# Performance work log

Measured on AMD Instinct MI355X. Metric: run time of the kernel, lower is better.

## Reference

```python
import jax, jax.numpy as jnp
import numpy as np

N = 100000      # nodes
E = 1600000     # edges
C_IN = 128
H = 64          # hidden_channels
FC = [128, 64, 32, 16]
G = 64          # graphs in batch
EPS = 1e-5


def _glorot(key, fan_in, fan_out):
    s = 1.0 / np.sqrt(fan_in)
    return jax.random.uniform(key, (fan_in, fan_out), jnp.float32, -s, s)


def setup_inputs() -> dict:
    key = jax.random.key(0)
    ks = jax.random.split(key, 24)
    inp = {
        "x": jax.random.normal(ks[0], (N, C_IN), jnp.float32),
        "edge_index": jax.random.randint(ks[1], (2, E), 0, N, jnp.int32),
        "batch": jnp.sort(jax.random.randint(ks[2], (N,), 0, G, jnp.int32)),
        # GCN layers
        "W1": _glorot(ks[3], C_IN, H), "b1": jnp.zeros((H,), jnp.float32),
        "W2": _glorot(ks[4], H, H),    "b2": jnp.zeros((H,), jnp.float32),
        # BatchNorm affine params
        "gamma1": jnp.ones((H,), jnp.float32), "beta1": jnp.zeros((H,), jnp.float32),
        "gamma2": jnp.ones((H,), jnp.float32), "beta2": jnp.zeros((H,), jnp.float32),
        # MLP stack 64->128->64->32->16->1
        "fW1": _glorot(ks[5], H, FC[0]),     "fb1": jnp.zeros((FC[0],), jnp.float32),
        "fW2": _glorot(ks[6], FC[0], FC[1]), "fb2": jnp.zeros((FC[1],), jnp.float32),
        "fW3": _glorot(ks[7], FC[1], FC[2]), "fb3": jnp.zeros((FC[2],), jnp.float32),
        "fW4": _glorot(ks[8], FC[2], FC[3]), "fb4": jnp.zeros((FC[3],), jnp.float32),
        "oW": _glorot(ks[9], FC[3], 1),      "ob": jnp.zeros((1,), jnp.float32),
    }
    return inp


def gcn_conv(x, W, b, src, dst):
    # x' = D^{-1/2} (A + I) D^{-1/2} X W + b   (PyG GCNConv, add_self_loops=True)
    h = x @ W                                             # [N, H]
    loops = jnp.arange(N, dtype=src.dtype)
    s = jnp.concatenate([src, loops])
    d = jnp.concatenate([dst, loops])
    deg = jax.ops.segment_sum(jnp.ones_like(d, jnp.float32), d, num_segments=N)
    dinv = jax.lax.rsqrt(deg)                             # deg >= 1 (self-loops)
    norm = dinv[s] * dinv[d]                              # [E+N]
    msg = h[s] * norm[:, None]                            # gather + scale
    return jax.ops.segment_sum(msg, d, num_segments=N) + b


def batch_norm(x, gamma, beta):
    mu = jnp.mean(x, axis=0)
    var = jnp.mean((x - mu) ** 2, axis=0)                 # biased, as torch BN
    return (x - mu) * jax.lax.rsqrt(var + EPS) * gamma + beta


def reference(x, edge_index, batch, W1, b1, W2, b2, gamma1, beta1, gamma2, beta2,
              fW1, fb1, fW2, fb2, fW3, fb3, fW4, fb4, oW, ob):
    src, dst = edge_index[0], edge_index[1]
    h = jax.nn.relu(gcn_conv(x, W1, b1, src, dst))
    h = batch_norm(h, gamma1, beta1)                      # dropout = identity (eval)
    h = jax.nn.relu(gcn_conv(h, W2, b2, src, dst))
    h = batch_norm(h, gamma2, beta2)
    # global mean pool over graphs
    sums = jax.ops.segment_sum(h, batch, num_segments=G)
    cnts = jax.ops.segment_sum(jnp.ones((N,), jnp.float32), batch, num_segments=G)
    g = sums / jnp.maximum(cnts, 1.0)[:, None]            # [G, H]
    g = jax.nn.relu(g @ fW1 + fb1)
    g = jax.nn.relu(g @ fW2 + fb2)
    g = jax.nn.relu(g @ fW3 + fb3)
    g = jax.nn.relu(g @ fW4 + fb4)
    return g @ oW + ob                                    # [G, 1]
```

## Files before the change

kernel.cpp:

```cpp
#include <hip/hip_runtime.h>
#include <hip/hip_bf16.h>
#include <hip/hip_fp16.h>

#define NNODES 100000
#define NEDGES 1600000
#define NGRAPH 64
#define NCOPY  32
#define NSLOT  8

#define CAP     48
#define NGEMM1  1563

#define PSH     9
#define PSZ2    512
#define NP2     196
#define PCAP    9216
#define EPB     4096
#define NBP1    391

__global__ __launch_bounds__(1024) void k_bucket(const int* __restrict__ ei,
                                                 unsigned* __restrict__ pstage,
                                                 unsigned* __restrict__ pcur) {
    const int tid = threadIdx.x;
    __shared__ unsigned lcnt[NP2];
    __shared__ unsigned lbase[NP2];
    if (tid < NP2) lcnt[tid] = 0u;
    __syncthreads();

    int e = blockIdx.x * EPB + tid * 4;
    bool valid = (e < NEDGES);
    unsigned v0=0,v1=0,v2=0,v3=0, p0=0,p1=0,p2=0,p3=0, o0=0,o1=0,o2=0,o3=0;
    if (valid) {
        int4 sv = *reinterpret_cast<const int4*>(&ei[e]);
        int4 dv = *reinterpret_cast<const int4*>(&ei[NEDGES + e]);
        unsigned d;
        d = (unsigned)dv.x; p0 = d >> PSH; v0 = ((d & (PSZ2-1u)) << 17) | (unsigned)sv.x; o0 = atomicAdd(&lcnt[p0], 1u);
        d = (unsigned)dv.y; p1 = d >> PSH; v1 = ((d & (PSZ2-1u)) << 17) | (unsigned)sv.y; o1 = atomicAdd(&lcnt[p1], 1u);
        d = (unsigned)dv.z; p2 = d >> PSH; v2 = ((d & (PSZ2-1u)) << 17) | (unsigned)sv.z; o2 = atomicAdd(&lcnt[p2], 1u);
        d = (unsigned)dv.w; p3 = d >> PSH; v3 = ((d & (PSZ2-1u)) << 17) | (unsigned)sv.w; o3 = atomicAdd(&lcnt[p3], 1u);
    }
    __syncthreads();
    if (tid < NP2) {
        unsigned c = lcnt[tid];
        lbase[tid] = c ? atomicAdd(&pcur[tid], c) : 0u;
    }
    __syncthreads();
    if (valid) {
        unsigned i0 = lbase[p0] + o0; if (i0 < PCAP) pstage[(size_t)p0 * PCAP + i0] = v0;
        unsigned i1 = lbase[p1] + o1; if (i1 < PCAP) pstage[(size_t)p1 * PCAP + i1] = v1;
        unsigned i2 = lbase[p2] + o2; if (i2 < PCAP) pstage[(size_t)p2 * PCAP + i2] = v2;
        unsigned i3 = lbase[p3] + o3; if (i3 < PCAP) pstage[(size_t)p3 * PCAP + i3] = v3;
    }
}

__global__ __launch_bounds__(1024) void k_build(const unsigned* __restrict__ pstage,
                                                const unsigned* __restrict__ pcur,
                                                unsigned* __restrict__ cnt,
                                                float* __restrict__ dinv,
                                                unsigned* __restrict__ colidx) {
    const int p   = blockIdx.x;
    const int tid = threadIdx.x;
    __shared__ unsigned cl[PSZ2];
    if (tid < PSZ2) cl[tid] = 0u;
    __syncthreads();
    unsigned nedge = min(pcur[p], (unsigned)PCAP);
    const unsigned* q = &pstage[(size_t)p * PCAP];
    for (unsigned i = tid; i < nedge; i += 1024) {
        unsigned v    = q[i];
        unsigned r    = v >> 17;
        unsigned src  = v & 0x1FFFFu;
        unsigned slot = atomicAdd(&cl[r], 1u);
        unsigned node = ((unsigned)p << PSH) + r;
        if (slot < CAP) colidx[node * CAP + slot] = src;
    }
    __syncthreads();
    if (tid < PSZ2) {
        unsigned node = ((unsigned)p << PSH) + (unsigned)tid;
        if (node < NNODES) {
            unsigned c = cl[tid];
            cnt[node]  = c;
            dinv[node] = rsqrtf((float)(c + 1u));
        }
    }
}

__global__ __launch_bounds__(256) void k_gemm1(const float* __restrict__ A,
                                               const float* __restrict__ W,
                                               const float* __restrict__ rowscale,
                                               __half* __restrict__ hd) {
    __shared__ float wlds[64 * 64];
    __shared__ float alds[64 * 68];
    const int tid = threadIdx.x;
    const int tc = (tid & 15) * 4;
    const int tr = (tid >> 4) * 4;
    const int row0 = blockIdx.x * 64;
    float acc[4][4];
    #pragma unroll
    for (int i = 0; i < 4; ++i)
        #pragma unroll
        for (int j = 0; j < 4; ++j) acc[i][j] = 0.f;

    for (int kc = 0; kc < 2; ++kc) {
        for (int idx2 = tid; idx2 < 64 * 16; idx2 += 256) {
            int r = idx2 >> 4, kk = (idx2 & 15) * 4;
            *reinterpret_cast<float4*>(&wlds[r * 64 + kk]) =
                *reinterpret_cast<const float4*>(&W[(kc * 64 + r) * 64 + kk]);
        }
        for (int idx2 = tid; idx2 < 64 * 16; idx2 += 256) {
            int r = idx2 >> 4, kk = (idx2 & 15) * 4;
            int row = row0 + r;
            float4 v = make_float4(0.f, 0.f, 0.f, 0.f);
            if (row < NNODES) v = *reinterpret_cast<const float4*>(&A[(size_t)row * 128 + kc * 64 + kk]);
            *reinterpret_cast<float4*>(&alds[r * 68 + kk]) = v;
        }
        __syncthreads();
        #pragma unroll 8
        for (int k = 0; k < 64; ++k) {
            float4 wv = *reinterpret_cast<const float4*>(&wlds[k * 64 + tc]);
            float av[4];
            #pragma unroll
            for (int i = 0; i < 4; ++i) av[i] = alds[(tr + i) * 68 + k];
            #pragma unroll
            for (int i = 0; i < 4; ++i) {
                acc[i][0] = fmaf(av[i], wv.x, acc[i][0]);
                acc[i][1] = fmaf(av[i], wv.y, acc[i][1]);
                acc[i][2] = fmaf(av[i], wv.z, acc[i][2]);
                acc[i][3] = fmaf(av[i], wv.w, acc[i][3]);
            }
        }
        __syncthreads();
    }
    #pragma unroll
    for (int i = 0; i < 4; ++i) {
        int row = row0 + tr + i;
        if (row < NNODES) {
            float f = rowscale[row];
            __half2* p = reinterpret_cast<__half2*>(&hd[(size_t)row * 64 + tc]);
            p[0] = __floats2half2_rn(acc[i][0] * f, acc[i][1] * f);
            p[1] = __floats2half2_rn(acc[i][2] * f, acc[i][3] * f);
        }
    }
}

__device__ __forceinline__ void acc_row(const __half* __restrict__ hd, unsigned s, int c0, float4& acc) {
    uint2 u = *reinterpret_cast<const uint2*>(&hd[(size_t)s * 64 + c0]);
    __half2 x01 = *reinterpret_cast<__half2*>(&u.x);
    __half2 x23 = *reinterpret_cast<__half2*>(&u.y);
    float2 f01 = __half22float2(x01);
    float2 f23 = __half22float2(x23);
    acc.x += f01.x; acc.y += f01.y; acc.z += f23.x; acc.w += f23.y;
}

#define WAVE_REDUCE_8(s0,s1,s2,s3,q0,q1,q2,q3)                      \
    {                                                                \
        _Pragma("unroll")                                            \
        for (int m = 16; m < 64; m <<= 1) {                          \
            s0 += __shfl_xor(s0, m); s1 += __shfl_xor(s1, m);        \
            s2 += __shfl_xor(s2, m); s3 += __shfl_xor(s3, m);        \
            q0 += __shfl_xor(q0, m); q1 += __shfl_xor(q1, m);        \
            q2 += __shfl_xor(q2, m); q3 += __shfl_xor(q3, m);        \
        }                                                            \
    }

__global__ __launch_bounds__(256) void k_gather_fused(const unsigned* __restrict__ cnt,
                                                      const unsigned* __restrict__ colidx,
                                                      const __half* __restrict__ hd,
                                                      const float* __restrict__ dinv,
                                                      const float* __restrict__ bias,
                                                      __half* __restrict__ acth,
                                                      float* bn_sum, float* bn_sq, int n) {
    const int tid = threadIdx.x;
    const int grp = tid >> 4;
    const int c0  = (tid & 15) * 4;
    float4 bv = *reinterpret_cast<const float4*>(&bias[c0]);
    float s0=0.f,s1=0.f,s2=0.f,s3=0.f, q0=0.f,q1=0.f,q2=0.f,q3=0.f;

    #pragma unroll
    for (int it = 0; it < 2; ++it) {
        int node = blockIdx.x * 32 + grp * 2 + it;
        if (node < n) {
            unsigned deg = cnt[node];
            unsigned lo = (unsigned)node * CAP;
            unsigned hi = lo + deg;
            float4 acc = make_float4(0.f, 0.f, 0.f, 0.f);
            acc_row(hd, (unsigned)node, c0, acc);
            unsigned j = lo;
            for (; j + 4 <= hi; j += 4) {
                uint4 a = *reinterpret_cast<const uint4*>(&colidx[j]);
                acc_row(hd, a.x, c0, acc);
                acc_row(hd, a.y, c0, acc);
                acc_row(hd, a.z, c0, acc);
                acc_row(hd, a.w, c0, acc);
            }
            for (; j < hi; ++j) acc_row(hd, colidx[j], c0, acc);
            float w = dinv[node];
            float4 r;
            r.x = fmaxf(fmaf(acc.x, w, bv.x), 0.f);
            r.y = fmaxf(fmaf(acc.y, w, bv.y), 0.f);
            r.z = fmaxf(fmaf(acc.z, w, bv.z), 0.f);
            r.w = fmaxf(fmaf(acc.w, w, bv.w), 0.f);
            __half2* pa = reinterpret_cast<__half2*>(&acth[(size_t)node * 64 + c0]);
            pa[0] = __floats2half2_rn(r.x, r.y);
            pa[1] = __floats2half2_rn(r.z, r.w);
            s0 += r.x; s1 += r.y; s2 += r.z; s3 += r.w;
            q0 = fmaf(r.x, r.x, q0); q1 = fmaf(r.y, r.y, q1);
            q2 = fmaf(r.z, r.z, q2); q3 = fmaf(r.w, r.w, q3);
        }
    }

    WAVE_REDUCE_8(s0,s1,s2,s3,q0,q1,q2,q3);
    __shared__ float ls[4 * 64];
    __shared__ float lq[4 * 64];
    int lane = tid & 63, wid = tid >> 6;
    if (lane < 16) {
        *reinterpret_cast<float4*>(&ls[wid * 64 + lane * 4]) = make_float4(s0, s1, s2, s3);
        *reinterpret_cast<float4*>(&lq[wid * 64 + lane * 4]) = make_float4(q0, q1, q2, q3);
    }
    __syncthreads();
    if (tid < 64) {
        int cpy = (blockIdx.x & (NCOPY - 1)) * 64;
        float S = ls[tid] + ls[64 + tid] + ls[128 + tid] + ls[192 + tid];
        float Q = lq[tid] + lq[64 + tid] + lq[128 + tid] + lq[192 + tid];
        atomicAdd(&bn_sum[cpy + tid], S);
        atomicAdd(&bn_sq[cpy + tid],  Q);
    }
}

__global__ __launch_bounds__(256) void k_gemm2_fold(const __half* __restrict__ A,
                                                    const float* __restrict__ W2,
                                                    const float* __restrict__ bn_sum,
                                                    const float* __restrict__ bn_sq,
                                                    const float* __restrict__ gamma,
                                                    const float* __restrict__ beta,
                                                    const float* __restrict__ rowscale,
                                                    __half* __restrict__ hd, int n) {
    __shared__ float wlds[64 * 64];
    __shared__ float alds[64 * 68];
    __shared__ float scs[64], shs[64], c2s[64];
    const int tid = threadIdx.x;
    const int tc  = (tid & 15) * 4;
    const int tr  = (tid >> 4) * 4;
    const int row0 = blockIdx.x * 64;

    if (tid < 64) {
        float S = 0.f, Q = 0.f;
        #pragma unroll
        for (int cpy = 0; cpy < NCOPY; ++cpy) { S += bn_sum[cpy * 64 + tid]; Q += bn_sq[cpy * 64 + tid]; }
        float inv_n = 1.0f / (float)n;
        float mu  = S * inv_n;
        float var = Q * inv_n - mu * mu;
        float s = gamma[tid] * rsqrtf(var + 1e-5f);
        scs[tid] = s; shs[tid] = beta[tid] - mu * s;
    }
    __syncthreads();
    for (int idx = tid; idx < 4096; idx += 256) {
        int k = idx >> 6;
        wlds[idx] = scs[k] * W2[idx];
    }
    if (tid < 64) {
        float acc = 0.f;
        for (int k = 0; k < 64; ++k) acc = fmaf(shs[k], W2[k * 64 + tid], acc);
        c2s[tid] = acc;
    }
    for (int idx = tid; idx < 64 * 16; idx += 256) {
        int r = idx >> 4, kk = (idx & 15) * 4;
        int row = row0 + r;
        float4 v = make_float4(0.f, 0.f, 0.f, 0.f);
        if (row < n) {
            uint2 u = *reinterpret_cast<const uint2*>(&A[(size_t)row * 64 + kk]);
            __half2 h01 = *reinterpret_cast<__half2*>(&u.x);
            __half2 h23 = *reinterpret_cast<__half2*>(&u.y);
            float2 f01 = __half22float2(h01);
            float2 f23 = __half22float2(h23);
            v = make_float4(f01.x, f01.y, f23.x, f23.y);
        }
        *reinterpret_cast<float4*>(&alds[r * 68 + kk]) = v;
    }
    __syncthreads();

    float acc[4][4];
    float4 cv = make_float4(c2s[tc], c2s[tc + 1], c2s[tc + 2], c2s[tc + 3]);
    #pragma unroll
    for (int i = 0; i < 4; ++i) { acc[i][0]=cv.x; acc[i][1]=cv.y; acc[i][2]=cv.z; acc[i][3]=cv.w; }

    #pragma unroll 8
    for (int k = 0; k < 64; ++k) {
        float4 wv = *reinterpret_cast<const float4*>(&wlds[k * 64 + tc]);
        float av[4];
        #pragma unroll
        for (int i = 0; i < 4; ++i) av[i] = alds[(tr + i) * 68 + k];
        #pragma unroll
        for (int i = 0; i < 4; ++i) {
            acc[i][0] = fmaf(av[i], wv.x, acc[i][0]);
            acc[i][1] = fmaf(av[i], wv.y, acc[i][1]);
            acc[i][2] = fmaf(av[i], wv.z, acc[i][2]);
            acc[i][3] = fmaf(av[i], wv.w, acc[i][3]);
        }
    }
    #pragma unroll
    for (int i = 0; i < 4; ++i) {
        int row = row0 + tr + i;
        if (row < n) {
            float f = rowscale[row];
            __half2* p = reinterpret_cast<__half2*>(&hd[(size_t)row * 64 + tc]);
            p[0] = __floats2half2_rn(acc[i][0] * f, acc[i][1] * f);
            p[1] = __floats2half2_rn(acc[i][2] * f, acc[i][3] * f);
        }
    }
}

__global__ __launch_bounds__(256) void k_gather_pool(const unsigned* __restrict__ cnt,
                                                     const unsigned* __restrict__ colidx,
                                                     const __half* __restrict__ hd,
                                                     const float* __restrict__ dinv,
                                                     const float* __restrict__ bias,
                                                     const int* __restrict__ batch,
                                                     float* __restrict__ gsum,
                                                     float* bn_sum, float* bn_sq, int n) {
    const int tid = threadIdx.x;
    const int grp = tid >> 4;
    const int c0  = (tid & 15) * 4;
    float4 bv = *reinterpret_cast<const float4*>(&bias[c0]);
    float s0=0.f,s1=0.f,s2=0.f,s3=0.f, q0=0.f,q1=0.f,q2=0.f,q3=0.f;

    __shared__ float lds_pool[NSLOT * 64];
    for (int i = tid; i < NSLOT * 64; i += 256) lds_pool[i] = 0.f;
    int node0 = blockIdx.x * 32;
    int g0 = batch[node0 < n ? node0 : (n - 1)];
    __syncthreads();

    #pragma unroll
    for (int it = 0; it < 2; ++it) {
        int node = node0 + grp * 2 + it;
        if (node < n) {
            unsigned deg = cnt[node];
            unsigned lo = (unsigned)node * CAP;
            unsigned hi = lo + deg;
            float4 acc = make_float4(0.f, 0.f, 0.f, 0.f);
            acc_row(hd, (unsigned)node, c0, acc);
            unsigned j = lo;
            for (; j + 4 <= hi; j += 4) {
                uint4 a = *reinterpret_cast<const uint4*>(&colidx[j]);
                acc_row(hd, a.x, c0, acc);
                acc_row(hd, a.y, c0, acc);
                acc_row(hd, a.z, c0, acc);
                acc_row(hd, a.w, c0, acc);
            }
            for (; j < hi; ++j) acc_row(hd, colidx[j], c0, acc);
            float w = dinv[node];
            float4 r;
            r.x = fmaxf(fmaf(acc.x, w, bv.x), 0.f);
            r.y = fmaxf(fmaf(acc.y, w, bv.y), 0.f);
            r.z = fmaxf(fmaf(acc.z, w, bv.z), 0.f);
            r.w = fmaxf(fmaf(acc.w, w, bv.w), 0.f);
            s0 += r.x; s1 += r.y; s2 += r.z; s3 += r.w;
            q0 = fmaf(r.x, r.x, q0); q1 = fmaf(r.y, r.y, q1);
            q2 = fmaf(r.z, r.z, q2); q3 = fmaf(r.w, r.w, q3);
            int slot = batch[node] - g0;
            if (slot < NSLOT) {
                atomicAdd(&lds_pool[slot * 64 + c0 + 0], r.x);
                atomicAdd(&lds_pool[slot * 64 + c0 + 1], r.y);
                atomicAdd(&lds_pool[slot * 64 + c0 + 2], r.z);
                atomicAdd(&lds_pool[slot * 64 + c0 + 3], r.w);
            } else {
                int g = g0 + slot;
                atomicAdd(&gsum[g * 64 + c0 + 0], r.x);
                atomicAdd(&gsum[g * 64 + c0 + 1], r.y);
                atomicAdd(&gsum[g * 64 + c0 + 2], r.z);
                atomicAdd(&gsum[g * 64 + c0 + 3], r.w);
            }
        }
    }

    WAVE_REDUCE_8(s0,s1,s2,s3,q0,q1,q2,q3);
    __shared__ float ls[4 * 64];
    __shared__ float lq[4 * 64];
    int lane = tid & 63, wid = tid >> 6;
    if (lane < 16) {
        *reinterpret_cast<float4*>(&ls[wid * 64 + lane * 4]) = make_float4(s0, s1, s2, s3);
        *reinterpret_cast<float4*>(&lq[wid * 64 + lane * 4]) = make_float4(q0, q1, q2, q3);
    }
    __syncthreads();
    if (tid < 64) {
        int cpy = (blockIdx.x & (NCOPY - 1)) * 64;
        float S = ls[tid] + ls[64 + tid] + ls[128 + tid] + ls[192 + tid];
        float Q = lq[tid] + lq[64 + tid] + lq[128 + tid] + lq[192 + tid];
        atomicAdd(&bn_sum[cpy + tid], S);
        atomicAdd(&bn_sq[cpy + tid],  Q);
        #pragma unroll
        for (int sl = 0; sl < NSLOT; ++sl) {
            int g = g0 + sl;
            if (g < NGRAPH) {
                float v = lds_pool[sl * 64 + tid];
                if (v != 0.f) atomicAdd(&gsum[g * 64 + tid], v);
            }
        }
    }
}

__device__ __forceinline__ int lower_bound_i(const int* a, int n, int v) {
    int lo = 0, hi = n;
    while (lo < hi) { int m = (lo + hi) >> 1; if (a[m] < v) lo = m + 1; else hi = m; }
    return lo;
}
__global__ __launch_bounds__(128) void k_mlp(const float* __restrict__ gsum,
                                             const int* __restrict__ batch, int n,
                                             const float* __restrict__ bn_sum, const float* __restrict__ bn_sq,
                                             const float* __restrict__ gamma, const float* __restrict__ beta,
                                             const float* __restrict__ fW1, const float* __restrict__ fb1,
                                             const float* __restrict__ fW2, const float* __restrict__ fb2,
                                             const float* __restrict__ fW3, const float* __restrict__ fb3,
                                             const float* __restrict__ fW4, const float* __restrict__ fb4,
                                             const float* __restrict__ oW,  const float* __restrict__ ob,
                                             float* __restrict__ out) {
    int g = blockIdx.x;
    int t = threadIdx.x;
    __shared__ float a[128], bbuf[128];
    if (t < 64) {
        float S = 0.f, Q = 0.f;
        #pragma unroll
        for (int cpy = 0; cpy < NCOPY; ++cpy) { S += bn_sum[cpy * 64 + t]; Q += bn_sq[cpy * 64 + t]; }
        float inv_n = 1.0f / (float)n;
        float mu  = S * inv_n;
        float var = Q * inv_n - mu * mu;
        float s   = gamma[t] * rsqrtf(var + 1e-5f);
        float sh  = beta[t] - mu * s;
        int lo = lower_bound_i(batch, n, g);
        int hi = lower_bound_i(batch, n, g + 1);
        int cnt = hi - lo;
        a[t] = (cnt > 0) ? (gsum[g * 64 + t] / (float)cnt) * s + sh : 0.f;
    }
    __syncthreads();
    {
        float acc = fb1[t];
        for (int k = 0; k < 64; ++k) acc = fmaf(a[k], fW1[k * 128 + t], acc);
        bbuf[t] = fmaxf(acc, 0.f);
    }
    __syncthreads();
    if (t < 64) {
        float acc = fb2[t];
        for (int k = 0; k < 128; ++k) acc = fmaf(bbuf[k], fW2[k * 64 + t], acc);
        a[t] = fmaxf(acc, 0.f);
    }
    __syncthreads();
    if (t < 32) {
        float acc = fb3[t];
        for (int k = 0; k < 64; ++k) acc = fmaf(a[k], fW3[k * 32 + t], acc);
        bbuf[t] = fmaxf(acc, 0.f);
    }
    __syncthreads();
    if (t < 16) {
        float acc = fb4[t];
        for (int k = 0; k < 32; ++k) acc = fmaf(bbuf[k], fW4[k * 16 + t], acc);
        a[t] = fmaxf(acc, 0.f);
    }
    __syncthreads();
    if (t == 0) {
        float acc = ob[0];
        for (int k = 0; k < 16; ++k) acc = fmaf(a[k], oW[k], acc);
        out[g] = acc;
    }
}

extern "C" void kernel_launch(void* const* d_in, const int* in_sizes, int n_in,
                              void* d_out, int out_size, void* d_ws, size_t ws_size,
                              hipStream_t stream) {
    const float* x      = (const float*)d_in[0];
    const int*   ei     = (const int*)  d_in[1];
    const int*   batch  = (const int*)  d_in[2];
    const float* W1     = (const float*)d_in[3];
    const float* b1     = (const float*)d_in[4];
    const float* W2     = (const float*)d_in[5];
    const float* b2     = (const float*)d_in[6];
    const float* gamma1 = (const float*)d_in[7];
    const float* beta1  = (const float*)d_in[8];
    const float* gamma2 = (const float*)d_in[9];
    const float* beta2  = (const float*)d_in[10];
    const float* fW1    = (const float*)d_in[11];
    const float* fb1    = (const float*)d_in[12];
    const float* fW2    = (const float*)d_in[13];
    const float* fb2    = (const float*)d_in[14];
    const float* fW3    = (const float*)d_in[15];
    const float* fb3    = (const float*)d_in[16];
    const float* fW4    = (const float*)d_in[17];
    const float* fb4    = (const float*)d_in[18];
    const float* oW     = (const float*)d_in[19];
    const float* ob     = (const float*)d_in[20];
    float* out = (float*)d_out;

    const int N = NNODES, G = NGRAPH;

    char* base = (char*)d_ws;
    __half*   hd     = (__half*)base;
    __half*   acth   = (__half*)(base + (size_t)N * 64 * 2);
    unsigned* cnt    = (unsigned*)(base + (size_t)N * 64 * 4);
    float*    dinv   = (float*)(cnt + N);
    unsigned* colidx = (unsigned*)(dinv + N);
    float*    bn1s   = (float*)(colidx + (size_t)N * CAP);
    float*    bn1q   = bn1s + NCOPY * 64;
    float*    bn2s   = bn1q + NCOPY * 64;
    float*    bn2q   = bn2s + NCOPY * 64;
    float*    gsum   = bn2q + NCOPY * 64;
    unsigned* pcur   = (unsigned*)(gsum + (size_t)G * 64);
    const size_t ZBYTES = (size_t)(4 * NCOPY * 64 + G * 64) * 4 + (size_t)NP2 * 4;
    unsigned* pstage = (unsigned*)acth;

    hipMemsetAsync(bn1s, 0, ZBYTES, stream);

    k_bucket<<<NBP1, 1024, 0, stream>>>(ei, pstage, pcur);

    k_build<<<NP2, 1024, 0, stream>>>(pstage, pcur, cnt, dinv, colidx);

    k_gemm1<<<NGEMM1, 256, 0, stream>>>(x, W1, dinv, hd);

    k_gather_fused<<<(N + 31) / 32, 256, 0, stream>>>(cnt, colidx, hd, dinv, b1, acth, bn1s, bn1q, N);

    k_gemm2_fold<<<NGEMM1, 256, 0, stream>>>(acth, W2, bn1s, bn1q, gamma1, beta1, dinv, hd, N);

    k_gather_pool<<<(N + 31) / 32, 256, 0, stream>>>(cnt, colidx, hd, dinv, b2, batch, gsum, bn2s, bn2q, N);

    k_mlp<<<G, 128, 0, stream>>>(gsum, batch, N, bn2s, bn2q, gamma2, beta2,
                                 fW1, fb1, fW2, fb2, fW3, fb3, fW4, fb4, oW, ob, out);
}
```

Baseline: 305.9 us.

## Merge memset, bucketing, CSR build and first GEMM into one cooperative kernel

Replaces the memset plus three separate launches (edge bucketing, per-partition CSR build, first-layer GEMM) with a single cooperative kernel that uses grid-wide syncs between phases and grid-stride loops. The zeroing of accumulators moves into the kernel. The GEMM phase is reworked for 1024-thread blocks, with each thread computing one row by four columns instead of a 4x4 tile. This is meant to remove launch gaps and memset overhead, at the cost of grid.sync barriers, lower per-thread GEMM reuse, and occupancy-limited grid sizing.

Result: slower. 654.7 us (+114.0%).

```diff
diff --git a/kernel.cpp b/kernel.cpp
--- a/kernel.cpp
+++ b/kernel.cpp
@@ -1,6 +1,9 @@
 #include <hip/hip_runtime.h>
+#include <hip/hip_cooperative_groups.h>
 #include <hip/hip_bf16.h>
 #include <hip/hip_fp16.h>
+
+namespace cg = cooperative_groups;
 
 #define NNODES 100000
 #define NEDGES 1600000
@@ -18,126 +21,123 @@
 #define EPB     4096
 #define NBP1    391
 
-__global__ __launch_bounds__(1024) void k_bucket(const int* __restrict__ ei,
-                                                 unsigned* __restrict__ pstage,
-                                                 unsigned* __restrict__ pcur) {
-    const int tid = threadIdx.x;
+__global__ __launch_bounds__(1024, 8) void k_front(const float* __restrict__ A,
+                                                   const float* __restrict__ W,
+                                                   const int* __restrict__ ei,
+                                                   unsigned* __restrict__ pstage,
+                                                   unsigned* __restrict__ pcur,
+                                                   unsigned* __restrict__ cnt,
+                                                   float* __restrict__ dinv,
+                                                   unsigned* __restrict__ colidx,
+                                                   float* __restrict__ zbase,
+                                                   int zwords,
+                                                   __half* __restrict__ hd) {
+    cg::grid_group grid = cg::this_grid();
+    const int tid  = threadIdx.x;
+    const int gdim = gridDim.x;
+
     __shared__ unsigned lcnt[NP2];
     __shared__ unsigned lbase[NP2];
-    if (tid < NP2) lcnt[tid] = 0u;
-    __syncthreads();
-
-    int e = blockIdx.x * EPB + tid * 4;
-    bool valid = (e < NEDGES);
-    unsigned v0=0,v1=0,v2=0,v3=0, p0=0,p1=0,p2=0,p3=0, o0=0,o1=0,o2=0,o3=0;
-    if (valid) {
-        int4 sv = *reinterpret_cast<const int4*>(&ei[e]);
-        int4 dv = *reinterpret_cast<const int4*>(&ei[NEDGES + e]);
-        unsigned d;
-        d = (unsigned)dv.x; p0 = d >> PSH; v0 = ((d & (PSZ2-1u)) << 17) | (unsigned)sv.x; o0 = atomicAdd(&lcnt[p0], 1u);
-        d = (unsigned)dv.y; p1 = d >> PSH; v1 = ((d & (PSZ2-1u)) << 17) | (unsigned)sv.y; o1 = atomicAdd(&lcnt[p1], 1u);
-        d = (unsigned)dv.z; p2 = d >> PSH; v2 = ((d & (PSZ2-1u)) << 17) | (unsigned)sv.z; o2 = atomicAdd(&lcnt[p2], 1u);
-        d = (unsigned)dv.w; p3 = d >> PSH; v3 = ((d & (PSZ2-1u)) << 17) | (unsigned)sv.w; o3 = atomicAdd(&lcnt[p3], 1u);
-    }
-    __syncthreads();
-    if (tid < NP2) {
-        unsigned c = lcnt[tid];
-        lbase[tid] = c ? atomicAdd(&pcur[tid], c) : 0u;
-    }
-    __syncthreads();
-    if (valid) {
-        unsigned i0 = lbase[p0] + o0; if (i0 < PCAP) pstage[(size_t)p0 * PCAP + i0] = v0;
-        unsigned i1 = lbase[p1] + o1; if (i1 < PCAP) pstage[(size_t)p1 * PCAP + i1] = v1;
-        unsigned i2 = lbase[p2] + o2; if (i2 < PCAP) pstage[(size_t)p2 * PCAP + i2] = v2;
-        unsigned i3 = lbase[p3] + o3; if (i3 < PCAP) pstage[(size_t)p3 * PCAP + i3] = v3;
-    }
-}
-
-__global__ __launch_bounds__(1024) void k_build(const unsigned* __restrict__ pstage,
-                                                const unsigned* __restrict__ pcur,
-                                                unsigned* __restrict__ cnt,
-                                                float* __restrict__ dinv,
-                                                unsigned* __restrict__ colidx) {
-    const int p   = blockIdx.x;
-    const int tid = threadIdx.x;
     __shared__ unsigned cl[PSZ2];
-    if (tid < PSZ2) cl[tid] = 0u;
-    __syncthreads();
-    unsigned nedge = min(pcur[p], (unsigned)PCAP);
-    const unsigned* q = &pstage[(size_t)p * PCAP];
-    for (unsigned i = tid; i < nedge; i += 1024) {
-        unsigned v    = q[i];
-        unsigned r    = v >> 17;
-        unsigned src  = v & 0x1FFFFu;
-        unsigned slot = atomicAdd(&cl[r], 1u);
-        unsigned node = ((unsigned)p << PSH) + r;
-        if (slot < CAP) colidx[node * CAP + slot] = src;
-    }
-    __syncthreads();
-    if (tid < PSZ2) {
-        unsigned node = ((unsigned)p << PSH) + (unsigned)tid;
-        if (node < NNODES) {
-            unsigned c = cl[tid];
-            cnt[node]  = c;
-            dinv[node] = rsqrtf((float)(c + 1u));
-        }
-    }
-}
-
-__global__ __launch_bounds__(256) void k_gemm1(const float* __restrict__ A,
-                                               const float* __restrict__ W,
-                                               const float* __restrict__ rowscale,
-                                               __half* __restrict__ hd) {
     __shared__ float wlds[64 * 64];
     __shared__ float alds[64 * 68];
-    const int tid = threadIdx.x;
-    const int tc = (tid & 15) * 4;
-    const int tr = (tid >> 4) * 4;
-    const int row0 = blockIdx.x * 64;
-    float acc[4][4];
-    #pragma unroll
-    for (int i = 0; i < 4; ++i)
-        #pragma unroll
-        for (int j = 0; j < 4; ++j) acc[i][j] = 0.f;
-
-    for (int kc = 0; kc < 2; ++kc) {
-        for (int idx2 = tid; idx2 < 64 * 16; idx2 += 256) {
-            int r = idx2 >> 4, kk = (idx2 & 15) * 4;
-            *reinterpret_cast<float4*>(&wlds[r * 64 + kk]) =
-                *reinterpret_cast<const float4*>(&W[(kc * 64 + r) * 64 + kk]);
-        }
-        for (int idx2 = tid; idx2 < 64 * 16; idx2 += 256) {
-            int r = idx2 >> 4, kk = (idx2 & 15) * 4;
-            int row = row0 + r;
-            float4 v = make_float4(0.f, 0.f, 0.f, 0.f);
-            if (row < NNODES) v = *reinterpret_cast<const float4*>(&A[(size_t)row * 128 + kc * 64 + kk]);
-            *reinterpret_cast<float4*>(&alds[r * 68 + kk]) = v;
-        }
-        __syncthreads();
-        #pragma unroll 8
-        for (int k = 0; k < 64; ++k) {
-            float4 wv = *reinterpret_cast<const float4*>(&wlds[k * 64 + tc]);
-            float av[4];
-            #pragma unroll
-            for (int i = 0; i < 4; ++i) av[i] = alds[(tr + i) * 68 + k];
-            #pragma unroll
-            for (int i = 0; i < 4; ++i) {
-                acc[i][0] = fmaf(av[i], wv.x, acc[i][0]);
-                acc[i][1] = fmaf(av[i], wv.y, acc[i][1]);
-                acc[i][2] = fmaf(av[i], wv.z, acc[i][2]);
-                acc[i][3] = fmaf(av[i], wv.w, acc[i][3]);
-            }
-        }
-        __syncthreads();
-    }
-    #pragma unroll
-    for (int i = 0; i < 4; ++i) {
-        int row = row0 + tr + i;
-        if (row < NNODES) {
-            float f = rowscale[row];
-            __half2* p = reinterpret_cast<__half2*>(&hd[(size_t)row * 64 + tc]);
-            p[0] = __floats2half2_rn(acc[i][0] * f, acc[i][1] * f);
-            p[1] = __floats2half2_rn(acc[i][2] * f, acc[i][3] * f);
+
+    for (int i = blockIdx.x * 1024 + tid; i < zwords; i += gdim * 1024) zbase[i] = 0.f;
+    grid.sync();
+
+    for (int s = blockIdx.x; s < NBP1; s += gdim) {
+        if (tid < NP2) lcnt[tid] = 0u;
+        __syncthreads();
+        int e = s * EPB + tid * 4;
+        bool valid = (e < NEDGES);
+        unsigned v0=0,v1=0,v2=0,v3=0, p0=0,p1=0,p2=0,p3=0, o0=0,o1=0,o2=0,o3=0;
+        if (valid) {
+            int4 sv = *reinterpret_cast<const int4*>(&ei[e]);
+            int4 dv = *reinterpret_cast<const int4*>(&ei[NEDGES + e]);
+            unsigned d;
+            d = (unsigned)dv.x; p0 = d >> PSH; v0 = ((d & (PSZ2-1u)) << 17) | (unsigned)sv.x; o0 = atomicAdd(&lcnt[p0], 1u);
+            d = (unsigned)dv.y; p1 = d >> PSH; v1 = ((d & (PSZ2-1u)) << 17) | (unsigned)sv.y; o1 = atomicAdd(&lcnt[p1], 1u);
+            d = (unsigned)dv.z; p2 = d >> PSH; v2 = ((d & (PSZ2-1u)) << 17) | (unsigned)sv.z; o2 = atomicAdd(&lcnt[p2], 1u);
+            d = (unsigned)dv.w; p3 = d >> PSH; v3 = ((d & (PSZ2-1u)) << 17) | (unsigned)sv.w; o3 = atomicAdd(&lcnt[p3], 1u);
+        }
+        __syncthreads();
+        if (tid < NP2) {
+            unsigned c = lcnt[tid];
+            lbase[tid] = c ? atomicAdd(&pcur[tid], c) : 0u;
+        }
+        __syncthreads();
+        if (valid) {
+            unsigned i0 = lbase[p0] + o0; if (i0 < PCAP) pstage[(size_t)p0 * PCAP + i0] = v0;
+            unsigned i1 = lbase[p1] + o1; if (i1 < PCAP) pstage[(size_t)p1 * PCAP + i1] = v1;
+            unsigned i2 = lbase[p2] + o2; if (i2 < PCAP) pstage[(size_t)p2 * PCAP + i2] = v2;
+            unsigned i3 = lbase[p3] + o3; if (i3 < PCAP) pstage[(size_t)p3 * PCAP + i3] = v3;
+        }
+        __syncthreads();
+    }
+    __threadfence();
+    grid.sync();
+
+    for (int p = blockIdx.x; p < NP2; p += gdim) {
+        if (tid < PSZ2) cl[tid] = 0u;
+        __syncthreads();
+        unsigned nedge = min(pcur[p], (unsigned)PCAP);
+        const unsigned* q = &pstage[(size_t)p * PCAP];
+        for (unsigned i = tid; i < nedge; i += 1024) {
+            unsigned v    = q[i];
+            unsigned r    = v >> 17;
+            unsigned src  = v & 0x1FFFFu;
+            unsigned slot = atomicAdd(&cl[r], 1u);
+            unsigned node = ((unsigned)p << PSH) + r;
+            if (slot < CAP) colidx[node * CAP + slot] = src;
+        }
+        __syncthreads();
+        if (tid < PSZ2) {
+            unsigned node = ((unsigned)p << PSH) + (unsigned)tid;
+            if (node < NNODES) {
+                unsigned c = cl[tid];
+                cnt[node]  = c;
+                dinv[node] = rsqrtf((float)(c + 1u));
+            }
+        }
+        __syncthreads();
+    }
+    __threadfence();
+    grid.sync();
+
+    {
+        const int rw = tid >> 4;
+        const int c4 = (tid & 15) * 4;
+        for (int t = blockIdx.x; t < NGEMM1; t += gdim) {
+            int row0 = t * 64;
+            float a0 = 0.f, a1 = 0.f, a2 = 0.f, a3 = 0.f;
+            for (int kc = 0; kc < 2; ++kc) {
+                *reinterpret_cast<float4*>(&wlds[rw * 64 + c4]) =
+                    *reinterpret_cast<const float4*>(&W[(kc * 64 + rw) * 64 + c4]);
+                {
+                    int rr = row0 + rw;
+                    float4 v = make_float4(0.f, 0.f, 0.f, 0.f);
+                    if (rr < NNODES) v = *reinterpret_cast<const float4*>(&A[(size_t)rr * 128 + kc * 64 + c4]);
+                    *reinterpret_cast<float4*>(&alds[rw * 68 + c4]) = v;
+                }
+                __syncthreads();
+                #pragma unroll 8
+                for (int k = 0; k < 64; ++k) {
+                    float av = alds[rw * 68 + k];
+                    float4 wv = *reinterpret_cast<const float4*>(&wlds[k * 64 + c4]);
+                    a0 = fmaf(av, wv.x, a0);
+                    a1 = fmaf(av, wv.y, a1);
+                    a2 = fmaf(av, wv.z, a2);
+                    a3 = fmaf(av, wv.w, a3);
+                }
+                __syncthreads();
+            }
+            int rr = row0 + rw;
+            if (rr < NNODES) {
+                float f = dinv[rr];
+                __half2* p = reinterpret_cast<__half2*>(&hd[(size_t)rr * 64 + c4]);
+                p[0] = __floats2half2_rn(a0 * f, a1 * f);
+                p[1] = __floats2half2_rn(a2 * f, a3 * f);
+            }
         }
     }
 }
@@ -502,16 +502,18 @@
     float*    bn2q   = bn2s + NCOPY * 64;
     float*    gsum   = bn2q + NCOPY * 64;
     unsigned* pcur   = (unsigned*)(gsum + (size_t)G * 64);
-    const size_t ZBYTES = (size_t)(4 * NCOPY * 64 + G * 64) * 4 + (size_t)NP2 * 4;
+    int zwords = 4 * NCOPY * 64 + G * 64 + NP2;
     unsigned* pstage = (unsigned*)acth;
-
-    hipMemsetAsync(bn1s, 0, ZBYTES, stream);
-
-    k_bucket<<<NBP1, 1024, 0, stream>>>(ei, pstage, pcur);
-
-    k_build<<<NP2, 1024, 0, stream>>>(pstage, pcur, cnt, dinv, colidx);
-
-    k_gemm1<<<NGEMM1, 256, 0, stream>>>(x, W1, dinv, hd);
+    float* zbase = bn1s;
+
+    int maxb = 0;
+    hipOccupancyMaxActiveBlocksPerMultiprocessor(&maxb, k_front, 1024, 0);
+    if (maxb < 1) maxb = 1;
+    int gfront = NBP1 < maxb * 256 ? NBP1 : maxb * 256;
+    void* fargs[] = { (void*)&x, (void*)&W1, (void*)&ei, (void*)&pstage, (void*)&pcur,
+                      (void*)&cnt, (void*)&dinv, (void*)&colidx, (void*)&zbase,
+                      (void*)&zwords, (void*)&hd };
+    hipLaunchCooperativeKernel((void*)k_front, dim3(gfront), dim3(1024), fargs, 0, stream);
 
     k_gather_fused<<<(N + 31) / 32, 256, 0, stream>>>(cnt, colidx, hd, dinv, b1, acth, bn1s, bn1q, N);
 
```
